# Kernel tuning notes

Measured on AMD Instinct MI355X. Metric: run time of the kernel, lower is better.

## Reference

```python
import jax, jax.numpy as jnp
import numpy as np

OUT_FEATURES = 11008
IN_FEATURES = 4096
BLOCK_SIZE = 128
NUM_BLOCKS = IN_FEATURES // BLOCK_SIZE  # 32
M_TOKENS = 4096  # flattened batch*seq


def _pack_int4(q):
    # q: int8 values in [-8, 7], flattened; pack 2 nibbles per int8 (matches pack_int4_to_int8)
    flat = q.reshape(-1)
    u = (flat.astype(jnp.int32) + 8).astype(jnp.uint8)
    packed = (u[0::2] | (u[1::2] << 4)).astype(jnp.int8)
    return packed


def _unpack_int4(packed, shape):
    # matches unpack_int8_to_int4
    pu = packed.astype(jnp.uint8)
    lower = pu & 15
    upper = (pu >> 4) & 15
    un = jnp.stack([lower, upper], axis=1).reshape(-1)
    n = int(np.prod(shape))
    un = un[:n].astype(jnp.int8) - 8
    return un.reshape(shape)


def setup_inputs() -> dict:
    key = jax.random.key(0)
    k_x, k_w, k_b = jax.random.split(key, 3)
    x = jax.random.normal(k_x, (M_TOKENS, IN_FEATURES), dtype=jnp.float32)
    w = jax.random.normal(k_w, (OUT_FEATURES, IN_FEATURES), dtype=jnp.float32) * 0.02
    bias = jax.random.normal(k_b, (OUT_FEATURES,), dtype=jnp.float32) * 0.01
    # blockwise symmetric 4-bit quantization (matches _quantize_blockwise)
    wr = w.reshape(OUT_FEATURES, NUM_BLOCKS, BLOCK_SIZE).transpose(1, 2, 0)  # (nb, bs, out)
    max_val = jnp.max(jnp.abs(wr), axis=1, keepdims=True)  # (nb, 1, out)
    qmax = 7.0
    scale3 = jnp.clip(max_val / qmax, 1e-8, None)
    q = jnp.clip(jnp.round(wr / scale3), -8, 7).astype(jnp.int8)  # (nb, bs, out)
    scale = scale3.squeeze(1)  # (nb, out)
    packed_w = _pack_int4(q)
    return {"x": x, "packed_w": packed_w, "scale": scale, "bias": bias}


def reference(x, packed_w, scale, bias):
    # unpack int4 nibbles -> (num_blocks, block_size, out)
    q = _unpack_int4(packed_w, (NUM_BLOCKS, BLOCK_SIZE, OUT_FEATURES))
    # dequantize with per-(block, out-channel) scale
    w_deq = q.astype(jnp.float32) * scale[:, None, :]  # (nb, bs, out)
    # y = x @ W^T + b, with x blocked along the in dimension
    xb = x.reshape(x.shape[0], NUM_BLOCKS, BLOCK_SIZE)
    y = jnp.einsum('mnb,nbo->mo', xb, w_deq) + bias
    return y
```

## Files before the change

### kernel.cpp

```cpp
#include <hip/hip_runtime.h>
#include <hip/hip_bf16.h>
#include <stdint.h>

#define NOUT 11008
#define KIN  4096
#define MTOK 4096
#define PLD  5504
#define NSTEP 128
#define NTN 43
#define NTM 16
#define ACHUNK 16384
#define BCHUNK 16384
#define WSA_BYTES ((size_t)NTM * NSTEP * ACHUNK)
#define WSW_BYTES ((size_t)NTN * NSTEP * BCHUNK)

typedef short bf16x8 __attribute__((ext_vector_type(8)));
typedef float f32x4  __attribute__((ext_vector_type(4)));

typedef __attribute__((address_space(3))) uint8_t lds_u8_t;
typedef __attribute__((address_space(1))) const uint8_t glb_u8_t;

__device__ __forceinline__ uint32_t bfpack(float lo, float hi){
    __hip_bfloat16 a = __float2bfloat16(lo);
    __hip_bfloat16 b = __float2bfloat16(hi);
    uint16_t ua, ub;
    __builtin_memcpy(&ua, &a, 2);
    __builtin_memcpy(&ub, &b, 2);
    return (uint32_t)ua | ((uint32_t)ub << 16);
}

__device__ __forceinline__ int swzA(int r){ return ((r >> 1) & 3) << 4; }

__global__ __launch_bounds__(256)
void prepA(const float* __restrict__ x, uint8_t* __restrict__ wsA)
{
    int gid = blockIdx.x * 256 + threadIdx.x;
    int m  = gid >> 10;
    int k  = (gid & 1023) << 2;
    float4 v = *reinterpret_cast<const float4*>(x + (size_t)m * KIN + k);
    uint32_t lo = bfpack(v.x, v.y), hi = bfpack(v.z, v.w);
    int mt = m >> 8, ml = m & 255, t = k >> 5, kl = k & 31;
    size_t dst = (size_t)(mt * NSTEP + t) * ACHUNK + ml * 64 + ((kl * 2) ^ swzA(ml));
    *reinterpret_cast<uint2*>(wsA + dst) = make_uint2(lo, hi);
}

__global__ __launch_bounds__(256)
void prepW2(const int32_t* __restrict__ pw, const float* __restrict__ sc,
            uint8_t* __restrict__ wsW)
{
    const int t  = blockIdx.x;
    const int nt = blockIdx.y;
    const int c  = threadIdx.x;
    const int col = nt * 256 + c;
    const int np  = col >> 1;
    const uint32_t sh = (uint32_t)(col & 1) * 4;
    const int32_t* p = pw + (size_t)(t * 32) * PLD + np;
    const float s  = sc[(size_t)(t >> 2) * NOUT + col];
    const float m8 = -8.f * s;
    uint8_t* out = wsW + ((size_t)nt * NSTEP + t) * BCHUNK + c * 64;
#pragma unroll
    for (int k8 = 0; k8 < 4; ++k8) {
        uint32_t r[4];
#pragma unroll
        for (int kk = 0; kk < 4; ++kk) {
            uint32_t w0 = (uint32_t)p[(size_t)(k8 * 8 + kk * 2)     * PLD];
            uint32_t w1 = (uint32_t)p[(size_t)(k8 * 8 + kk * 2 + 1) * PLD];
            float f0 = fmaf((float)((w0 >> sh) & 15u), s, m8);
            float f1 = fmaf((float)((w1 >> sh) & 15u), s, m8);
            r[kk] = bfpack(f0, f1);
        }
        *reinterpret_cast<uint4*>(out + ((k8 * 16) ^ swzA(c))) = *reinterpret_cast<uint4*>(r);
    }
}

__global__ __launch_bounds__(512, 1)
void qlin_gemm12(const uint8_t* __restrict__ wsA, const uint8_t* __restrict__ wsW,
                 const float* __restrict__ bias, float* __restrict__ y)
{
    __shared__ __align__(16) uint8_t ldsA[4][ACHUNK];
    __shared__ __align__(16) uint8_t ldsB[4][BCHUNK];

    const int tid  = threadIdx.x;
    const int lane = tid & 63;
    const int wid  = tid >> 6;
    const int wr = wid >> 2, wc = wid & 3;

    const int lb = (blockIdx.x & 7) * 86 + (blockIdx.x >> 3);
    const int mt = lb / NTN, nt = lb % NTN;
    const int m0 = mt * 256, n0 = nt * 256;

    const int cl = lane & 15;
    const int k8 = lane >> 4;

    int aOff[8];
#pragma unroll
    for (int i = 0; i < 8; ++i) {
        int ml = wr * 128 + i * 16 + cl;
        aOff[i] = ml * 64 + ((k8 * 16) ^ swzA(ml));
    }
    int bOff[4];
#pragma unroll
    for (int j = 0; j < 4; ++j) {
        int cc = wc * 64 + j * 16 + cl;
        bOff[j] = cc * 64 + ((k8 * 16) ^ swzA(cc));
    }

    const uint8_t* wsAbase = wsA + (size_t)mt * NSTEP * ACHUNK;
    const uint8_t* wsWbase = wsW + (size_t)nt * NSTEP * BCHUNK;

    f32x4 acc[8][4];
#pragma unroll
    for (int i = 0; i < 8; ++i)
#pragma unroll
        for (int j = 0; j < 4; ++j)
            acc[i][j] = (f32x4){0.f, 0.f, 0.f, 0.f};

    bf16x8 af[4], bfr[4];

#define STAGE_A(buf, t) do { \
    const uint8_t* g_ = wsAbase + (size_t)(t) * ACHUNK + tid * 16; \
    __builtin_amdgcn_global_load_lds((glb_u8_t*)(g_),        (lds_u8_t*)(&ldsA[buf][tid*16]),        16, 0, 0); \
    __builtin_amdgcn_global_load_lds((glb_u8_t*)(g_ + 8192), (lds_u8_t*)(&ldsA[buf][tid*16 + 8192]), 16, 0, 0); \
} while(0)

#define STAGE_B(buf, t) do { \
    const uint8_t* g_ = wsWbase + (size_t)(t) * BCHUNK + tid * 16; \
    __builtin_amdgcn_global_load_lds((glb_u8_t*)(g_),        (lds_u8_t*)(&ldsB[buf][tid*16]),        16, 0, 0); \
    __builtin_amdgcn_global_load_lds((glb_u8_t*)(g_ + 8192), (lds_u8_t*)(&ldsB[buf][tid*16 + 8192]), 16, 0, 0); \
} while(0)

#define BAR() do { \
    asm volatile("" ::: "memory"); \
    __builtin_amdgcn_s_barrier(); \
    asm volatile("" ::: "memory"); \
} while(0)

#define PH_O(cb, sb, st) do { \
    STAGE_A(sb, st); \
    _Pragma("unroll") \
    for (int i = 0; i < 4; ++i) { \
        af[i]  = *reinterpret_cast<const bf16x8*>(ldsA[cb] + aOff[i]); \
        bfr[i] = *reinterpret_cast<const bf16x8*>(ldsB[cb] + bOff[i]); \
    } \
    BAR(); \
    __builtin_amdgcn_s_setprio(1); \
    _Pragma("unroll") \
    for (int j = 0; j < 4; ++j) { _Pragma("unroll") \
        for (int i = 0; i < 4; ++i) \
            acc[i][j] = __builtin_amdgcn_mfma_f32_16x16x32_bf16(af[i], bfr[j], acc[i][j], 0, 0, 0); } \
    __builtin_amdgcn_s_setprio(0); \
    BAR(); \
} while(0)

#define PH_E(cb, sb, st) do { \
    STAGE_B(sb, st); \
    _Pragma("unroll") \
    for (int i = 0; i < 4; ++i) af[i] = *reinterpret_cast<const bf16x8*>(ldsA[cb] + aOff[4 + i]); \
    BAR(); \
    __builtin_amdgcn_s_setprio(1); \
    _Pragma("unroll") \
    for (int j = 0; j < 4; ++j) { _Pragma("unroll") \
        for (int i = 0; i < 4; ++i) \
            acc[4 + i][j] = __builtin_amdgcn_mfma_f32_16x16x32_bf16(af[i], bfr[j], acc[4 + i][j], 0, 0, 0); } \
    __builtin_amdgcn_s_setprio(0); \
    asm volatile("s_waitcnt vmcnt(8)" ::: "memory"); \
    __builtin_amdgcn_sched_barrier(0); \
    BAR(); \
} while(0)

    STAGE_A(0, 0); STAGE_B(0, 0);
    STAGE_A(1, 1); STAGE_B(1, 1);
    STAGE_A(2, 2); STAGE_B(2, 2);
    asm volatile("s_waitcnt vmcnt(8)" ::: "memory");
    __builtin_amdgcn_sched_barrier(0);
    BAR();

#pragma unroll 1
    for (int tb = 0; tb < NSTEP; tb += 4) {
        const int s4 = (tb + 4 < NSTEP) ? tb + 4 : NSTEP - 1;
        const int s5 = (tb + 5 < NSTEP) ? tb + 5 : NSTEP - 1;
        const int s6 = (tb + 6 < NSTEP) ? tb + 6 : NSTEP - 1;
        PH_O(0, 3, tb + 3);  PH_E(0, 3, tb + 3);
        PH_O(1, 0, s4);      PH_E(1, 0, s4);
        PH_O(2, 1, s5);      PH_E(2, 1, s5);
        PH_O(3, 2, s6);      PH_E(3, 2, s6);
    }

    float bv[4];
#pragma unroll
    for (int j = 0; j < 4; ++j) bv[j] = bias[n0 + wc * 64 + j * 16 + cl];
    const int rg = (lane >> 4) * 4;
#pragma unroll
    for (int i = 0; i < 8; ++i) {
        const int mrow = m0 + wr * 128 + i * 16 + rg;
#pragma unroll
        for (int r = 0; r < 4; ++r) {
            float* yp = y + (size_t)(mrow + r) * NOUT + n0 + wc * 64 + cl;
#pragma unroll
            for (int j = 0; j < 4; ++j)
                yp[j * 16] = acc[i][j][r] + bv[j];
        }
    }

#undef STAGE_A
#undef STAGE_B
#undef BAR
#undef PH_O
#undef PH_E
}

extern "C" void kernel_launch(void* const* d_in, const int* in_sizes, int n_in,
                              void* d_out, int out_size, void* d_ws, size_t ws_size,
                              hipStream_t stream)
{
    const float*   xin  = (const float*)d_in[0];
    const int32_t* pw   = (const int32_t*)d_in[1];
    const float*   scal = (const float*)d_in[2];
    const float*   bias = (const float*)d_in[3];
    float* y = (float*)d_out;

    uint8_t* wsA = (uint8_t*)d_ws;
    uint8_t* wsW = wsA + WSA_BYTES;

    prepA<<<dim3((MTOK * (KIN / 4)) / 256), 256, 0, stream>>>(xin, wsA);
    prepW2<<<dim3(NSTEP, NTN), 256, 0, stream>>>(pw, scal, wsW);
    qlin_gemm12<<<dim3(NTM * NTN), 512, 0, stream>>>(wsA, wsW, bias, y);
}
```

Measured before the change: 416.3 us.

## Load B fragments directly from global into registers, double-buffered

The weight operand is no longer staged through LDS. Each wave reads its B fragments straight from global memory into a register double buffer one step ahead, and only A stays in LDS. This halves LDS usage and removes the LDS reads for B. The cost is that each of the four waves sharing a column tile issues redundant global loads, and the vmcnt accounting shifts to cover the in-flight register loads, so global latency may show up on the critical path.

```diff
diff --git a/kernel.cpp b/kernel.cpp
--- a/kernel.cpp
+++ b/kernel.cpp
@@ -31,6 +31,8 @@
 
 __device__ __forceinline__ int swzA(int r){ return ((r >> 1) & 3) << 4; }
 
+__device__ __forceinline__ int imin(int a, int b){ return a < b ? a : b; }
+
 __global__ __launch_bounds__(256)
 void prepA(const float* __restrict__ x, uint8_t* __restrict__ wsA)
 {
@@ -74,11 +76,10 @@
 }
 
 __global__ __launch_bounds__(512, 1)
-void qlin_gemm12(const uint8_t* __restrict__ wsA, const uint8_t* __restrict__ wsW,
+void qlin_gemm14(const uint8_t* __restrict__ wsA, const uint8_t* __restrict__ wsW,
                  const float* __restrict__ bias, float* __restrict__ y)
 {
     __shared__ __align__(16) uint8_t ldsA[4][ACHUNK];
-    __shared__ __align__(16) uint8_t ldsB[4][BCHUNK];
 
     const int tid  = threadIdx.x;
     const int lane = tid & 63;
@@ -115,7 +116,7 @@
         for (int j = 0; j < 4; ++j)
             acc[i][j] = (f32x4){0.f, 0.f, 0.f, 0.f};
 
-    bf16x8 af[4], bfr[4];
+    bf16x8 af[4], BFa[4], BFb[4];
 
 #define STAGE_A(buf, t) do { \
     const uint8_t* g_ = wsAbase + (size_t)(t) * ACHUNK + tid * 16; \
@@ -123,10 +124,10 @@
     __builtin_amdgcn_global_load_lds((glb_u8_t*)(g_ + 8192), (lds_u8_t*)(&ldsA[buf][tid*16 + 8192]), 16, 0, 0); \
 } while(0)
 
-#define STAGE_B(buf, t) do { \
-    const uint8_t* g_ = wsWbase + (size_t)(t) * BCHUNK + tid * 16; \
-    __builtin_amdgcn_global_load_lds((glb_u8_t*)(g_),        (lds_u8_t*)(&ldsB[buf][tid*16]),        16, 0, 0); \
-    __builtin_amdgcn_global_load_lds((glb_u8_t*)(g_ + 8192), (lds_u8_t*)(&ldsB[buf][tid*16 + 8192]), 16, 0, 0); \
+#define LOADB(BF, tn) do { \
+    const uint8_t* gb_ = wsWbase + (size_t)(tn) * BCHUNK; \
+    _Pragma("unroll") \
+    for (int j = 0; j < 4; ++j) BF[j] = *reinterpret_cast<const bf16x8*>(gb_ + bOff[j]); \
 } while(0)
 
 #define BAR() do { \
@@ -135,25 +136,22 @@
     asm volatile("" ::: "memory"); \
 } while(0)
 
-#define PH_O(cb, sb, st) do { \
+#define PH_O(cb, sb, st, BFC, BFN, tn) do { \
     STAGE_A(sb, st); \
-    _Pragma("unroll") \
-    for (int i = 0; i < 4; ++i) { \
-        af[i]  = *reinterpret_cast<const bf16x8*>(ldsA[cb] + aOff[i]); \
-        bfr[i] = *reinterpret_cast<const bf16x8*>(ldsB[cb] + bOff[i]); \
-    } \
+    LOADB(BFN, tn); \
+    _Pragma("unroll") \
+    for (int i = 0; i < 4; ++i) af[i] = *reinterpret_cast<const bf16x8*>(ldsA[cb] + aOff[i]); \
     BAR(); \
     __builtin_amdgcn_s_setprio(1); \
     _Pragma("unroll") \
     for (int j = 0; j < 4; ++j) { _Pragma("unroll") \
         for (int i = 0; i < 4; ++i) \
-            acc[i][j] = __builtin_amdgcn_mfma_f32_16x16x32_bf16(af[i], bfr[j], acc[i][j], 0, 0, 0); } \
+            acc[i][j] = __builtin_amdgcn_mfma_f32_16x16x32_bf16(af[i], BFC[j], acc[i][j], 0, 0, 0); } \
     __builtin_amdgcn_s_setprio(0); \
     BAR(); \
 } while(0)
 
-#define PH_E(cb, sb, st) do { \
-    STAGE_B(sb, st); \
+#define PH_E(cb, BFC) do { \
     _Pragma("unroll") \
     for (int i = 0; i < 4; ++i) af[i] = *reinterpret_cast<const bf16x8*>(ldsA[cb] + aOff[4 + i]); \
     BAR(); \
@@ -161,29 +159,31 @@
     _Pragma("unroll") \
     for (int j = 0; j < 4; ++j) { _Pragma("unroll") \
         for (int i = 0; i < 4; ++i) \
-            acc[4 + i][j] = __builtin_amdgcn_mfma_f32_16x16x32_bf16(af[i], bfr[j], acc[4 + i][j], 0, 0, 0); } \
+            acc[4 + i][j] = __builtin_amdgcn_mfma_f32_16x16x32_bf16(af[i], BFC[j], acc[4 + i][j], 0, 0, 0); } \
     __builtin_amdgcn_s_setprio(0); \
-    asm volatile("s_waitcnt vmcnt(8)" ::: "memory"); \
+    asm volatile("s_waitcnt vmcnt(12)" ::: "memory"); \
     __builtin_amdgcn_sched_barrier(0); \
     BAR(); \
 } while(0)
 
-    STAGE_A(0, 0); STAGE_B(0, 0);
-    STAGE_A(1, 1); STAGE_B(1, 1);
-    STAGE_A(2, 2); STAGE_B(2, 2);
+    STAGE_A(0, 0);
+    STAGE_A(1, 1);
+    STAGE_A(2, 2);
+    LOADB(BFa, 0);
     asm volatile("s_waitcnt vmcnt(8)" ::: "memory");
     __builtin_amdgcn_sched_barrier(0);
     BAR();
 
 #pragma unroll 1
     for (int tb = 0; tb < NSTEP; tb += 4) {
-        const int s4 = (tb + 4 < NSTEP) ? tb + 4 : NSTEP - 1;
-        const int s5 = (tb + 5 < NSTEP) ? tb + 5 : NSTEP - 1;
-        const int s6 = (tb + 6 < NSTEP) ? tb + 6 : NSTEP - 1;
-        PH_O(0, 3, tb + 3);  PH_E(0, 3, tb + 3);
-        PH_O(1, 0, s4);      PH_E(1, 0, s4);
-        PH_O(2, 1, s5);      PH_E(2, 1, s5);
-        PH_O(3, 2, s6);      PH_E(3, 2, s6);
+        { const int st = imin(tb + 3, 127), tn = imin(tb + 1, 127);
+          PH_O(0, 3, st, BFa, BFb, tn);  PH_E(0, BFa); }
+        { const int st = imin(tb + 4, 127), tn = imin(tb + 2, 127);
+          PH_O(1, 0, st, BFb, BFa, tn);  PH_E(1, BFb); }
+        { const int st = imin(tb + 5, 127), tn = imin(tb + 3, 127);
+          PH_O(2, 1, st, BFa, BFb, tn);  PH_E(2, BFa); }
+        { const int st = imin(tb + 6, 127), tn = imin(tb + 4, 127);
+          PH_O(3, 2, st, BFb, BFa, tn);  PH_E(3, BFb); }
     }
 
     float bv[4];
@@ -203,7 +203,7 @@
     }
 
 #undef STAGE_A
-#undef STAGE_B
+#undef LOADB
 #undef BAR
 #undef PH_O
 #undef PH_E
@@ -224,5 +224,5 @@
 
     prepA<<<dim3((MTOK * (KIN / 4)) / 256), 256, 0, stream>>>(xin, wsA);
     prepW2<<<dim3(NSTEP, NTN), 256, 0, stream>>>(pw, scal, wsW);
-    qlin_gemm12<<<dim3(NTM * NTN), 512, 0, stream>>>(wsA, wsW, bias, y);
-}
+    qlin_gemm14<<<dim3(NTM * NTN), 512, 0, stream>>>(wsA, wsW, bias, y);
+}
```

Result: slower. 477.9 us (+14.8%).
